# Performance work log

Hardware: AMD Instinct MI355X
Metric: run time of the kernel (lower is better)

The kernel has to match this reference:

```python
import jax, jax.numpy as jnp
import numpy as np

LN_EPS = 1e-5
GN_EPS = 0.00064
H_HEADS = 14
N_LAYER = 2

FLOATS = ["emb","ln0_w","ln0_b","ln1_w","ln1_b","ln2_w","ln2_b",
          "x_r","x_w","x_k","x_v","x_a","x_g",
          "w0","w1","w2","a0","a1","a2","v0","v1","v2","g1","g2",
          "k_k","k_a","r_k","Wr","Wk","Wv","Wo","lnx_w","lnx_b",
          "f_xk","f_key","f_val","lnout_w","lnout_b","head_w"]


def _ln(x, w, b):
    m = x.mean(-1, keepdims=True)
    v = jnp.var(x, axis=-1, keepdims=True)
    return (x - m) / jnp.sqrt(v + LN_EPS) * w + b


def _shift(x):
    # ZeroPad2d((0,0,1,-1)): token t sees token t-1, zeros at t=0
    return jnp.pad(x, ((0, 0), (1, 0), (0, 0)))[:, :-1]


def _group_norm(x, w, b, H):
    B, T, C = x.shape
    N = C // H
    xg = x.reshape(B, T, H, N)
    m = xg.mean(-1, keepdims=True)
    v = jnp.var(xg, axis=-1, keepdims=True)
    xg = (xg - m) / jnp.sqrt(v + GN_EPS)
    return xg.reshape(B, T, C) * w + b


def _rwkv7(r, w_raw, k, v, a, b, H):
    # WindBackstepping math: S_t = S_{t-1}*diag(exp(-exp(w))) + (S_{t-1} a) b^T + v k^T ; y_t = S_t r
    B, T, C = r.shape
    N = C // H
    rs = lambda t: jnp.swapaxes(t.reshape(B, T, H, N), 0, 1)  # [T,B,H,N]
    decay = jnp.exp(-jnp.exp(w_raw))
    xs = (rs(r), rs(decay), rs(k), rs(v), rs(a), rs(b))
    s0 = jnp.zeros((B, H, N, N), r.dtype)

    def step(s, inp):
        r_t, d_t, k_t, v_t, a_t, b_t = inp
        sa = jnp.einsum('bhij,bhj->bhi', s, a_t)
        s = s * d_t[:, :, None, :] + sa[..., None] * b_t[:, :, None, :] + v_t[..., None] * k_t[:, :, None, :]
        y = jnp.einsum('bhij,bhj->bhi', s, r_t)
        return s, y

    _, ys = jax.lax.scan(step, s0, xs)
    return jnp.swapaxes(ys, 0, 1).reshape(B, T, C)


def _forward(idx, P):
    H, L = H_HEADS, N_LAYER
    x = P["emb"][idx]  # [B,T,C]
    B, T, C = x.shape
    N = C // H
    v_first = jnp.zeros_like(x)
    for l in range(L):
        if l == 0:
            x = _ln(x, P["ln0_w"], P["ln0_b"])
        # --- time mix (RWKV_Tmix_x070) ---
        xn = _ln(x, P["ln1_w"][l], P["ln1_b"][l])
        xx = _shift(xn) - xn
        xr = xn + xx * P["x_r"][l]; xw = xn + xx * P["x_w"][l]
        xk = xn + xx * P["x_k"][l]; xv = xn + xx * P["x_v"][l]
        xa = xn + xx * P["x_a"][l]; xg = xn + xx * P["x_g"][l]
        r = xr @ P["Wr"][l]
        w = -jax.nn.softplus(-(P["w0"][l] + jnp.tanh(xw @ P["w1"][l]) @ P["w2"][l])) - 0.5
        k = xk @ P["Wk"][l]
        v = xv @ P["Wv"][l]
        if l == 0:
            v_first = v
        else:
            v = v + (v_first - v) * jax.nn.sigmoid(P["v0"][l] + (xv @ P["v1"][l]) @ P["v2"][l])
        a = jax.nn.sigmoid(P["a0"][l] + (xa @ P["a1"][l]) @ P["a2"][l])
        g = jax.nn.sigmoid(xg @ P["g1"][l]) @ P["g2"][l]
        kk = k * P["k_k"][l]
        kkh = kk.reshape(B, T, H, N)
        kk = (kkh / jnp.maximum(jnp.linalg.norm(kkh, axis=-1, keepdims=True), 1e-12)).reshape(B, T, C)
        k = k * (1.0 + (a - 1.0) * P["k_a"][l])
        y = _rwkv7(r, w, k, v, -kk, kk * a, H)
        y = _group_norm(y, P["lnx_w"][l], P["lnx_b"][l], H)
        rk = (r.reshape(B, T, H, N) * k.reshape(B, T, H, N) * P["r_k"][l]).sum(-1, keepdims=True)
        y = y + (rk * v.reshape(B, T, H, N)).reshape(B, T, C)
        x = x + (y * g) @ P["Wo"][l]
        # --- channel mix (RWKV_CMix_x070) ---
        xn2 = _ln(x, P["ln2_w"][l], P["ln2_b"][l])
        dx = _shift(xn2) - xn2
        kx = xn2 + dx * P["f_xk"][l]
        h = jnp.square(jax.nn.relu(kx @ P["f_key"][l]))
        x = x + h @ P["f_val"][l]
    x = _ln(x, P["lnout_w"], P["lnout_b"])
    return x @ P["head_w"]


def setup_inputs() -> dict:
    C, H, L = 896, 14, 2
    V, B, T = 32000, 4, 512
    D, DG, F4 = 64, 160, 4 * C  # LoRA dims per code formulas for C=896
    key = jax.random.key(0)
    ks = jax.random.split(key, 64)
    it = iter(range(64))

    def rn(shape, s=0.02):
        return jax.random.normal(ks[next(it)], shape, jnp.float32) * s

    def ru(shape):
        return jax.random.uniform(ks[next(it)], shape, dtype=jnp.float32)

    inp = {
        "idx": jax.random.randint(ks[next(it)], (B, T), 0, V),
        "emb": rn((V, C), 0.5),
        "ln0_w": jnp.ones((C,), jnp.float32), "ln0_b": jnp.zeros((C,), jnp.float32),
        "ln1_w": jnp.ones((L, C), jnp.float32), "ln1_b": jnp.zeros((L, C), jnp.float32),
        "ln2_w": jnp.ones((L, C), jnp.float32), "ln2_b": jnp.zeros((L, C), jnp.float32),
        "x_r": ru((L, C)), "x_w": ru((L, C)), "x_k": ru((L, C)),
        "x_v": ru((L, C)), "x_a": ru((L, C)), "x_g": ru((L, C)),
        "w0": rn((L, C), 1.0) - 2.0, "w1": rn((L, C, D)), "w2": rn((L, D, C), 0.1),
        "a0": rn((L, C), 0.1), "a1": rn((L, C, D)), "a2": rn((L, D, C), 0.1),
        "v0": rn((L, C), 0.1) + 0.73, "v1": rn((L, C, D)), "v2": rn((L, D, C), 0.1),
        "g1": rn((L, C, DG)), "g2": rn((L, DG, C), 0.1),
        "k_k": rn((L, C), 0.1) + 0.71, "k_a": rn((L, C), 0.02) + 1.02,
        "r_k": rn((L, H, C // H), 0.1) - 0.04,
        "Wr": rn((L, C, C)), "Wk": rn((L, C, C)), "Wv": rn((L, C, C)), "Wo": rn((L, C, C)),
        "lnx_w": jnp.ones((L, C), jnp.float32), "lnx_b": jnp.zeros((L, C), jnp.float32),
        "f_xk": ru((L, C)),
        "f_key": rn((L, C, F4)), "f_val": rn((L, F4, C)),
        "lnout_w": jnp.ones((C,), jnp.float32), "lnout_b": jnp.zeros((C,), jnp.float32),
        "head_w": rn((C, 1)),
    }
    return inp


def reference(idx, emb, ln0_w, ln0_b, ln1_w, ln1_b, ln2_w, ln2_b, x_r, x_w, x_k, x_v, x_a, x_g, w0, w1, w2, a0, a1, a2, v0, v1, v2, g1, g2, k_k, k_a, r_k, Wr, Wk, Wv, Wo, lnx_w, lnx_b, f_xk, f_key, f_val, lnout_w, lnout_b, head_w):
    vals = [emb, ln0_w, ln0_b, ln1_w, ln1_b, ln2_w, ln2_b, x_r, x_w, x_k, x_v, x_a, x_g, w0, w1, w2, a0, a1, a2, v0, v1, v2, g1, g2, k_k, k_a, r_k, Wr, Wk, Wv, Wo, lnx_w, lnx_b, f_xk, f_key, f_val, lnout_w, lnout_b, head_w]
    return _forward(idx, dict(zip(FLOATS, vals)))
```

## Files before the change

### kernel.cpp

```cpp
#include <hip/hip_runtime.h>
#include <hip/hip_bf16.h>
#include <math.h>

#define CC 896
#define TT 512
#define BB 4
#define HH 14
#define NN 64
#define DD 64
#define DGG 160
#define FF4 3584
#define MM (BB*TT)
#define RD 8
#define NCH 16
#define CL 32

typedef __attribute__((ext_vector_type(8))) short bf16x8;
typedef __attribute__((ext_vector_type(4))) float f32x4;

__device__ __forceinline__ float waveRedSum(float x) {
#pragma unroll
  for (int off = 32; off > 0; off >>= 1) x += __shfl_xor(x, off, 64);
  return x;
}

__device__ __forceinline__ float sigmoidf_(float x) { return 1.f / (1.f + expf(-x)); }

__device__ __forceinline__ ushort bf16bits(float v) {
  __hip_bfloat16 h = __float2bfloat16(v);
  return *(ushort*)&h;
}

__device__ __forceinline__ void gload_lds16(const void* g, void* l) {
  __builtin_amdgcn_global_load_lds((const __attribute__((address_space(1))) void*)g,
                                   (__attribute__((address_space(3))) void*)l, 16, 0, 0);
}
// ... 138 lines not shown
__device__ __forceinline__ void convT_body(const float* __restrict__ W,
                                           __hip_bfloat16* __restrict__ Wt,
                                           int K, int N, int KP, int NP,
                                           int bx, int by)
{
  __shared__ float tile[32][33];
  int bn = bx * 32, bk = by * 32;
  int tx = threadIdx.x & 31, ty = threadIdx.x >> 5;
#pragma unroll
  for (int i = 0; i < 4; i++) {
    int k = bk + ty + i * 8, n = bn + tx;
    tile[ty + i * 8][tx] = (k < K && n < N) ? W[(size_t)k * N + n] : 0.f;
  }
  __syncthreads();
#pragma unroll
  for (int i = 0; i < 4; i++) {
    int n = bn + ty + i * 8, k = bk + tx;
    if (n < NP && k < KP)
      Wt[(size_t)n * KP + k] = __float2bfloat16(tile[tx][ty + i * 8]);
  }
}

__global__ __launch_bounds__(256)
void convT_batch(const float* Wr, const float* Wk, const float* Wv, const float* Wo,
                 const float* a1, const float* a2, const float* v1, const float* v2,
                 const float* g1, const float* g2, const float* w1, const float* w2,
                 __hip_bfloat16* WrT, __hip_bfloat16* WkT, __hip_bfloat16* WvT,
                 __hip_bfloat16* WoT, __hip_bfloat16* a1T, __hip_bfloat16* a2T,
                 __hip_bfloat16* v1T, __hip_bfloat16* v2T, __hip_bfloat16* g1T,
                 __hip_bfloat16* g2T, __hip_bfloat16* w1T, __hip_bfloat16* w2T)
{
  const float* W; __hip_bfloat16* Wt; int K, N, KP, NP;
  switch (blockIdx.z) {
    case 0:  W = Wr; Wt = WrT; K = CC;  N = CC;  KP = CC;  NP = CC;  break;
    case 1:  W = Wk; Wt = WkT; K = CC;  N = CC;  KP = CC;  NP = CC;  break;
    case 2:  W = Wv; Wt = WvT; K = CC;  N = CC;  KP = CC;  NP = CC;  break;
    case 3:  W = Wo; Wt = WoT; K = CC;  N = CC;  KP = CC;  NP = CC;  break;
    case 4:  W = a1; Wt = a1T; K = CC;  N = DD;  KP = CC;  NP = DD;  break;
    case 5:  W = a2; Wt = a2T; K = DD;  N = CC;  KP = DD;  NP = CC;  break;
    case 6:  W = v1; Wt = v1T; K = CC;  N = DD;  KP = CC;  NP = DD;  break;
    case 7:  W = v2; Wt = v2T; K = DD;  N = CC;  KP = DD;  NP = CC;  break;
    case 8:  W = g1; Wt = g1T; K = CC;  N = DGG; KP = CC;  NP = 192; break;
    case 9:  W = g2; Wt = g2T; K = DGG; N = CC;  KP = 192; NP = CC;  break;
    case 10: W = w1; Wt = w1T; K = CC;  N = DD;  KP = CC;  NP = DD;  break;
    default: W = w2; Wt = w2T; K = DD;  N = CC;  KP = DD;  NP = CC;  break;
  }
  if ((int)blockIdx.x * 32 >= NP || (int)blockIdx.y * 32 >= KP) return;
  convT_body(W, Wt, K, N, KP, NP, blockIdx.x, blockIdx.y);
}

__global__ __launch_bounds__(256)
void convT_big(const float* fk, const float* fv,
               __hip_bfloat16* fkT, __hip_bfloat16* fvT)
{
  if (blockIdx.z == 0)
    convT_body(fk, fkT, CC, FF4, CC, FF4, blockIdx.x, blockIdx.y);
  else
    convT_body(fv, fvT, FF4, CC, FF4, CC, blockIdx.y, blockIdx.x);
}

template<int BN>
__device__ __forceinline__ void gemm_body(const __hip_bfloat16* __restrict__ A,
    const __hip_bfloat16* __restrict__ Bt, float* __restrict__ C,
    __hip_bfloat16* __restrict__ Cbf, int N, int K, const float* __restrict__ bias,
    const float* __restrict__ aux0, const float* __restrict__ aux1, int Nreal,
    int bx, int by, int epi)
{
  constexpr int WN = BN / 64;
  constexpr int WM = 4 / WN;
  constexpr int ROWS = 128 / WM;
  constexpr int MI = ROWS / 16;
  constexpr int BUF = (128 + BN) * 64;
  __shared__ __align__(16) ushort ldsu[2 * BUF];
  int tid = threadIdx.x;
  int lane = tid & 63, wave = tid >> 6;
  int wm, wn;
  if constexpr (WN == 2) { wm = wave >> 1; wn = wave & 1; } else { wm = wave; wn = 0; }
  int fl = lane & 15, fh = lane >> 4;
  int row0 = by * 128, col0 = bx * BN;

  const char* Abase = (const char*)A + (size_t)row0 * (size_t)(K * 2);
  const char* Bbase = (const char*)Bt + (size_t)col0 * (size_t)(K * 2);

  f32x4 acc[MI][4];
#pragma unroll
  for (int mi = 0; mi < MI; mi++)
#pragma unroll
    for (int ni = 0; ni < 4; ni++)
      acc[mi][ni] = (f32x4){0.f, 0.f, 0.f, 0.f};

  int srow = tid >> 3;
  int scol = (tid & 7) << 4;
  int ldsw = (wave << 10);

  auto stage = [&](int p, int k0) {
    char* AsB = (char*)(ldsu + p * BUF);
// ... 76 lines not shown
      int row = idx / BN;
      int col = idx - row * BN;
      float4 v4 = *(const float4*)&ldsu[idx];
      *(float4*)((char*)Cbf + ((size_t)(row0 + row) * N + col0 + col) * 2) = v4;
    }
  } else {
#pragma unroll
    for (int mi = 0; mi < MI; mi++) {
      int crow0 = row0 + wm * ROWS + mi * 16 + fh * 4;
#pragma unroll
      for (int ni = 0; ni < 4; ni++) {
        int ccol = col0 + wn * 64 + ni * 16 + fl;
#pragma unroll
        for (int e = 0; e < 4; e++) {
          size_t off = (size_t)(crow0 + e) * N + ccol;
          float v = acc[mi][ni][e];
          switch (epi) {
            case 0: C[off] = v; break;
            case 1: C[off] += v; break;
            case 5: C[off] = sigmoidf_(bias[ccol] + v); break;
            case 6: { float sg = sigmoidf_(bias[ccol] + v);
                      float vv = aux0[off];
                      C[off] = vv + (aux1[off] - vv) * sg; } break;
            default: { float z_ = bias[ccol] + v;
                       float sp_ = fmaxf(-z_, 0.f) + log1pf(expf(-fabsf(z_)));
                       C[off] = expf(-expf(-sp_ - 0.5f)); } break;
          }
        }
      }
    }
  }
}

template<int BN>
__global__ __launch_bounds__(256)
void gemm_ep(const __hip_bfloat16* __restrict__ A, const __hip_bfloat16* __restrict__ Bt,
             float* __restrict__ C, __hip_bfloat16* __restrict__ Cbf,
             int N, int K, const float* __restrict__ bias,
             const float* __restrict__ aux0, const float* __restrict__ aux1,
             int Nreal, int epi)
{
  gemm_body<BN>(A, Bt, C, Cbf, N, K, bias, aux0, aux1, Nreal, blockIdx.x, blockIdx.y, epi);
}

__global__ __launch_bounds__(256)
void gemm_rkv(const __hip_bfloat16* Ar, const __hip_bfloat16* Ak, const __hip_bfloat16* Av,
              const __hip_bfloat16* Br, const __hip_bfloat16* Bk, const __hip_bfloat16* Bv,
              float* Cr, float* Ck, float* Cv)
{
  const __hip_bfloat16* A; const __hip_bfloat16* Bt; float* C;
  if (blockIdx.z == 0)      { A = Ar; Bt = Br; C = Cr; }
  else if (blockIdx.z == 1) { A = Ak; Bt = Bk; C = Ck; }
  else                      { A = Av; Bt = Bv; C = Cv; }
  gemm_body<128>(A, Bt, C, nullptr, CC, CC, nullptr, nullptr, nullptr, CC,
                 blockIdx.x, blockIdx.y, 0);
}

__global__ __launch_bounds__(256)
void lora1_batch(const __hip_bfloat16* mixw, const __hip_bfloat16* mixa,
                 const __hip_bfloat16* mixv, const __hip_bfloat16* mixg,
                 const __hip_bfloat16* w1T, const __hip_bfloat16* a1T,
                 const __hip_bfloat16* v1T, const __hip_bfloat16* g1T,
                 __hip_bfloat16* t64w, __hip_bfloat16* t64a,
                 __hip_bfloat16* t64v, __hip_bfloat16* t160)
{
  int z = blockIdx.x;
  const __hip_bfloat16 *A, *Bt; __hip_bfloat16* Cbf; int N, epi, bx, Nreal;
  if (z == 0)      { A = mixw; Bt = w1T; Cbf = t64w; N = 64;  epi = 8; bx = 0; Nreal = 64; }
  else if (z == 1) { A = mixa; Bt = a1T; Cbf = t64a; N = 64;  epi = 3; bx = 0; Nreal = 64; }
  else if (z == 2) { A = mixv; Bt = v1T; Cbf = t64v; N = 64;  epi = 3; bx = 0; Nreal = 64; }
  else             { A = mixg; Bt = g1T; Cbf = t160; N = 192; epi = 4; bx = z - 3; Nreal = DGG; }
  gemm_body<64>(A, Bt, nullptr, Cbf, N, CC, nullptr, nullptr, nullptr, Nreal,
                bx, blockIdx.y, epi);
}

__global__ __launch_bounds__(256)
void lora2_batch(const __hip_bfloat16* t64w, const __hip_bfloat16* t64a,
                 const __hip_bfloat16* t160, const __hip_bfloat16* t64v,
                 const __hip_bfloat16* w2T, const __hip_bfloat16* a2T,
                 const __hip_bfloat16* g2T, const __hip_bfloat16* v2T,
                 float* dcy, float* ab, float* gb, float* vb,
                 const float* w0l, const float* a0l, const float* v0l,
                 const float* vfirst)
{
  int z = blockIdx.z;
  const __hip_bfloat16 *A, *Bt; float* C; const float* bias;
  const float *ax0, *ax1; int K, epi;
  if (z == 0)      { A = t64w; Bt = w2T; C = dcy; bias = w0l; K = 64;  epi = 7; ax0 = nullptr; ax1 = nullptr; }
  else if (z == 1) { A = t64a; Bt = a2T; C = ab;  bias = a0l; K = 64;  epi = 5; ax0 = nullptr; ax1 = nullptr; }
  else if (z == 2) { A = t160; Bt = g2T; C = gb;  bias = nullptr; K = 192; epi = 0; ax0 = nullptr; ax1 = nullptr; }
  else             { A = t64v; Bt = v2T; C = vb;  bias = v0l; K = 64;  epi = 6; ax0 = vb; ax1 = vfirst; }
  gemm_body<128>(A, Bt, C, nullptr, CC, K, bias, ax0, ax1, CC, blockIdx.x, blockIdx.y, epi);
}

__global__ __launch_bounds__(896)
void prep_kernel(const float* __restrict__ k_in, const float* __restrict__ a,
                 const float* __restrict__ k_k, const float* __restrict__ k_a,
                 float* __restrict__ kout, float* __restrict__ ain, float* __restrict__ bin)
{
  int m = blockIdx.x;
  int c = threadIdx.x;
  size_t off = (size_t)m * CC + c;
  float kv = k_in[off];
  float av = a[off];
  float kkv = kv * k_k[c];
  float ss = waveRedSum(kkv * kkv);
  float norm = sqrtf(ss);
  float kkn = kkv / fmaxf(norm, 1e-12f);
  ain[off] = -kkn;
  bin[off] = kkn * av;
  kout[off] = kv * (1.f + (av - 1.f) * k_a[c]);
}

__global__ __launch_bounds__(256)
void scanp1_kernel(const float* __restrict__ rp, const float* __restrict__ dp,
                   const float* __restrict__ kp, const float* __restrict__ vp,
                   const float* __restrict__ ap, const float* __restrict__ bp_,
                   float* __restrict__ yp, float* __restrict__ ubuf,
                   float* __restrict__ Pc, float* __restrict__ Zc)
{
  int bid = blockIdx.x;
  int bh = bid >> 4, c = bid & 15;
  int b = bh / HH, h = bh - b * HH;
  int tid = threadIdx.x, lane = tid & 63, w = tid >> 6;
  int w16 = w * 16;
  __shared__ __align__(16) float ring[RD][6][64];
  __shared__ float sa_part[2][4][64];
  __shared__ float pa_part[2][4][64];
  __shared__ float y_part[2][4][64];
  __shared__ float u_part[2][4][64];

  float s[16], p[16];
#pragma unroll
  for (int jj = 0; jj < 16; jj++) {
    s[jj] = 0.f;
    p[jj] = (lane == w16 + jj) ? 1.f : 0.f;
  }
  size_t base = ((size_t)b * TT + (size_t)c * CL) * CC + (size_t)h * NN + lane;

  const float* gA = nullptr; const float* gB = nullptr; int slA = 0, slB = 0;
  if (w == 1)      { gA = rp;  slA = 0; gB = dp;  slB = 1; }
  else if (w == 2) { gA = kp;  slA = 2; gB = vp;  slB = 5; }
  else if (w == 3) { gA = ap;  slA = 3; gB = bp_; slB = 4; }

  if (w) {
    for (int t0 = 0; t0 < RD; t0++) {
      gload_lds4(gA + base + (size_t)t0 * CC, &ring[t0][slA][0]);
      gload_lds4(gB + base + (size_t)t0 * CC, &ring[t0][slB][0]);
    }
    asm volatile("s_waitcnt vmcnt(0)" ::: "memory");
  }
  __builtin_amdgcn_s_barrier();
  __builtin_amdgcn_sched_barrier(0);

  for (int t = 0; t < CL; ++t) {
    int Pp = t & 1, Qp = Pp ^ 1;
    int slot = t & (RD - 1);
    float av[16], dv[16], kv[16], bv[16], rv[16];
#pragma unroll
    for (int q = 0; q < 4; q++) {
      *(float4*)&av[q * 4] = *(const float4*)&ring[slot][3][w16 + q * 4];
      *(float4*)&dv[q * 4] = *(const float4*)&ring[slot][1][w16 + q * 4];
      *(float4*)&kv[q * 4] = *(const float4*)&ring[slot][2][w16 + q * 4];
      *(float4*)&bv[q * 4] = *(const float4*)&ring[slot][4][w16 + q * 4];
      *(float4*)&rv[q * 4] = *(const float4*)&ring[slot][0][w16 + q * 4];
    }
    float vi = ring[slot][5][lane];
    float sp0 = 0.f, sp1 = 0.f, pp0 = 0.f, pp1 = 0.f;
#pragma unroll
    for (int jj = 0; jj < 8; jj++) {
      sp0 = fmaf(s[jj],     av[jj],     sp0);
      sp1 = fmaf(s[jj + 8], av[jj + 8], sp1);
      pp0 = fmaf(p[jj],     av[jj],     pp0);
      pp1 = fmaf(p[jj + 8], av[jj + 8], pp1);
    }
    sa_part[Pp][w][lane] = sp0 + sp1;
    pa_part[Pp][w][lane] = pp0 + pp1;
    if (w) { asm volatile("s_waitcnt vmcnt(12)" ::: "memory"); }
    asm volatile("s_waitcnt lgkmcnt(0)" ::: "memory");
    __builtin_amdgcn_s_barrier();
    __builtin_amdgcn_sched_barrier(0);
    if (w && t + RD < CL) {
      gload_lds4(gA + base + (size_t)(t + RD) * CC, &ring[slot][slA][0]);
      gload_lds4(gB + base + (size_t)(t + RD) * CC, &ring[slot][slB][0]);
    }
    if (w == 0 && t > 0) {
      float yo = (y_part[Qp][0][lane] + y_part[Qp][1][lane])
               + (y_part[Qp][2][lane] + y_part[Qp][3][lane]);
      yp[base + (size_t)(t - 1) * CC] = yo;
      float uo = (u_part[Qp][0][lane] + u_part[Qp][1][lane])
               + (u_part[Qp][2][lane] + u_part[Qp][3][lane]);
      ubuf[((size_t)bid * CL + (t - 1)) * 64 + lane] = uo;
    }
    float sa = (sa_part[Pp][0][lane] + sa_part[Pp][1][lane])
             + (sa_part[Pp][2][lane] + sa_part[Pp][3][lane]);
    float pa = (pa_part[Pp][0][lane] + pa_part[Pp][1][lane])
             + (pa_part[Pp][2][lane] + pa_part[Pp][3][lane]);
    float y0 = 0.f, y1 = 0.f, u0 = 0.f, u1 = 0.f;
#pragma unroll
    for (int jj = 0; jj < 8; jj++) {
      s[jj]     = fmaf(s[jj],     dv[jj],     fmaf(sa, bv[jj],     vi * kv[jj]));
      y0 = fmaf(s[jj], rv[jj], y0);
      s[jj + 8] = fmaf(s[jj + 8], dv[jj + 8], fmaf(sa, bv[jj + 8], vi * kv[jj + 8]));
      y1 = fmaf(s[jj + 8], rv[jj + 8], y1);
      p[jj]     = fmaf(p[jj],     dv[jj],     pa * bv[jj]);
      u0 = fmaf(p[jj], rv[jj], u0);
      p[jj + 8] = fmaf(p[jj + 8], dv[jj + 8], pa * bv[jj + 8]);
      u1 = fmaf(p[jj + 8], rv[jj + 8], u1);
    }
    y_part[Pp][w][lane] = y0 + y1;
    u_part[Pp][w][lane] = u0 + u1;
  }

  asm volatile("s_waitcnt lgkmcnt(0)" ::: "memory");
  __builtin_amdgcn_s_barrier();
  if (w == 0) {
    int Pl = (CL - 1) & 1;
    float yo = (y_part[Pl][0][lane] + y_part[Pl][1][lane])
             + (y_part[Pl][2][lane] + y_part[Pl][3][lane]);
    yp[base + (size_t)(CL - 1) * CC] = yo;
    float uo = (u_part[Pl][0][lane] + u_part[Pl][1][lane])
             + (u_part[Pl][2][lane] + u_part[Pl][3][lane]);
    ubuf[((size_t)bid * CL + (CL - 1)) * 64 + lane] = uo;
  }
  float* zp = Zc + ((size_t)bid * 64 + lane) * 64 + w16;
  float* pq = Pc + ((size_t)bid * 64 + lane) * 64 + w16;
#pragma unroll
  for (int q = 0; q < 4; q++) {
    *(float4*)&zp[q * 4] = make_float4(s[q*4], s[q*4+1], s[q*4+2], s[q*4+3]);
    *(float4*)&pq[q * 4] = make_float4(p[q*4], p[q*4+1], p[q*4+2], p[q*4+3]);
  }
}

__global__ __launch_bounds__(512)
void scanp2_kernel(const float* __restrict__ Pc, const float* __restrict__ Zc,
                   float* __restrict__ Sin)
{
  int bh = blockIdx.x;
  int tid = threadIdx.x;
  int i = tid & 63, jg = tid >> 6, j0 = jg * 8;
  int sr = tid >> 3, sq = (tid & 7) * 8;
  __shared__ float S_lds[64][65];
  __shared__ __align__(16) float P_lds[64][68];

#pragma unroll
  for (int jj = 0; jj < 8; jj++) S_lds[i][j0 + jj] = 0.f;

  size_t b0 = (size_t)bh * NCH * 4096;
  float4 pr0 = *(const float4*)(Pc + b0 + (size_t)sr * 64 + sq);
  float4 pr1 = *(const float4*)(Pc + b0 + (size_t)sr * 64 + sq + 4);

  for (int c = 0; c < NCH; c++) {
    size_t bidc = (size_t)bh * NCH + c;
// ... 117 lines not shown
  const float* v1     = (const float*)d_in[21];
  const float* v2     = (const float*)d_in[22];
  const float* g1     = (const float*)d_in[23];
  const float* g2     = (const float*)d_in[24];
  const float* k_k    = (const float*)d_in[25];
  const float* k_a    = (const float*)d_in[26];
  const float* r_k    = (const float*)d_in[27];
  const float* Wr     = (const float*)d_in[28];
  const float* Wk     = (const float*)d_in[29];
  const float* Wv     = (const float*)d_in[30];
  const float* Wo     = (const float*)d_in[31];
  const float* lnx_w  = (const float*)d_in[32];
  const float* lnx_b  = (const float*)d_in[33];
  const float* f_xk   = (const float*)d_in[34];
  const float* f_key  = (const float*)d_in[35];
  const float* f_val  = (const float*)d_in[36];
  const float* lnout_w = (const float*)d_in[37];
  const float* lnout_b = (const float*)d_in[38];
  const float* head_w  = (const float*)d_in[39];
  float* out = (float*)d_out;

  const size_t MC = (size_t)MM * CC;
  const size_t W2 = (size_t)CC * CC;
  float* ws   = (float*)d_ws;
  float* x      = ws;
  float* vfirst = x + MC;
  float* rb     = vfirst + MC;
  float* dcy    = rb + MC;
  float* kb     = dcy + MC;
  float* vb     = kb + MC;
  float* ab     = vb + MC;
  float* gb     = ab + MC;
  float* ainb   = gb + MC;
  float* binb   = ainb + MC;
  float* yb     = binb + MC;
  float* ubuf   = yb + MC;
  float* Pcb    = ubuf + MC;
  float* Zcb    = Pcb + 2 * MC;
  float* Sinb   = Zcb + 2 * MC;
  float* fend   = Sinb + 2 * MC;

  __hip_bfloat16* mixr_bf = (__hip_bfloat16*)fend;
  __hip_bfloat16* mixw_bf = mixr_bf + MC;
  __hip_bfloat16* mixk_bf = mixw_bf + MC;
  __hip_bfloat16* mixv_bf = mixk_bf + MC;
  __hip_bfloat16* mixa_bf = mixv_bf + MC;
  __hip_bfloat16* mixg_bf = mixa_bf + MC;
  __hip_bfloat16* WrT = mixg_bf + MC;
  __hip_bfloat16* WkT = WrT + W2;
  __hip_bfloat16* WvT = WkT + W2;
  __hip_bfloat16* WoT = WvT + W2;
  __hip_bfloat16* fkT = WoT + W2;
  __hip_bfloat16* fvT = fkT + (size_t)FF4 * CC;
  __hip_bfloat16* w1T = fvT + (size_t)FF4 * CC;
  __hip_bfloat16* a1T = w1T + (size_t)DD * CC;
  __hip_bfloat16* v1T = a1T + (size_t)DD * CC;
  __hip_bfloat16* w2T = v1T + (size_t)DD * CC;
  __hip_bfloat16* a2T = w2T + (size_t)DD * CC;
  __hip_bfloat16* v2T = a2T + (size_t)DD * CC;
  __hip_bfloat16* g1T = v2T + (size_t)DD * CC;
  __hip_bfloat16* g2T = g1T + (size_t)192 * CC;
  __hip_bfloat16* t64w = g2T + (size_t)192 * CC;
  __hip_bfloat16* t64a = t64w + (size_t)MM * 64;
  __hip_bfloat16* t64v = t64a + (size_t)MM * 64;
  __hip_bfloat16* t160 = t64v + (size_t)MM * 64;
  __hip_bfloat16* h_bf  = (__hip_bfloat16*)rb;
  __hip_bfloat16* yg_bf = (__hip_bfloat16*)ab;

  dim3 blk(256);

  ln_kernel<<<MM, blk, 0, stream>>>(emb, idx, ln0_w, ln0_b, x);

  for (int l = 0; l < 2; l++) {
    const float* Wr_l = Wr + (size_t)l * W2;
    const float* Wk_l = Wk + (size_t)l * W2;
    const float* Wv_l = Wv + (size_t)l * W2;
    const float* Wo_l = Wo + (size_t)l * W2;
    const float* w1_l = w1 + (size_t)l * CC * DD;
    const float* w2_l = w2 + (size_t)l * DD * CC;
    const float* a1_l = a1 + (size_t)l * CC * DD;
    const float* a2_l = a2 + (size_t)l * DD * CC;
    const float* v1_l = v1 + (size_t)l * CC * DD;
    const float* v2_l = v2 + (size_t)l * DD * CC;
    const float* g1_l = g1 + (size_t)l * CC * DGG;
    const float* g2_l = g2 + (size_t)l * DGG * CC;
    const float* fk_l = f_key + (size_t)l * CC * FF4;
    const float* fv_l = f_val + (size_t)l * FF4 * CC;

    convT_batch<<<dim3(28, 28, 12), blk, 0, stream>>>(
        Wr_l, Wk_l, Wv_l, Wo_l, a1_l, a2_l, v1_l, v2_l, g1_l, g2_l, w1_l, w2_l,
        WrT, WkT, WvT, WoT, a1T, a2T, v1T, v2T, g1T, g2T, w1T, w2T);
    convT_big<<<dim3(112, 28, 2), blk, 0, stream>>>(fk_l, fv_l, fkT, fvT);

    lnmix6_kernel<<<MM, blk, 0, stream>>>(x, ln1_w + l * CC, ln1_b + l * CC,
        x_r + l * CC, x_w + l * CC, x_k + l * CC, x_v + l * CC, x_a + l * CC, x_g + l * CC,
        mixr_bf, mixw_bf, mixk_bf, mixv_bf, mixa_bf, mixg_bf);

    gemm_rkv<<<dim3(7, 16, 3), blk, 0, stream>>>(mixr_bf, mixk_bf, mixv_bf,
                                                 WrT, WkT, WvT, rb, kb, vb);
    if (l == 0)
      hipMemcpyAsync(vfirst, vb, MC * sizeof(float), hipMemcpyDeviceToDevice, stream);

    lora1_batch<<<dim3(6, 16), blk, 0, stream>>>(mixw_bf, mixa_bf, mixv_bf, mixg_bf,
                                                 w1T, a1T, v1T, g1T,
                                                 t64w, t64a, t64v, t160);
    lora2_batch<<<dim3(7, 16, l == 0 ? 3 : 4), blk, 0, stream>>>(
        t64w, t64a, t160, t64v, w2T, a2T, g2T, v2T,
        dcy, ab, gb, vb, w0 + l * CC, a0 + l * CC, v0 + l * CC, vfirst);

    prep_kernel<<<MM, dim3(896), 0, stream>>>(kb, ab, k_k + l * CC, k_a + l * CC,
                                              kb, ainb, binb);
    scanp1_kernel<<<BB * HH * NCH, blk, 0, stream>>>(rb, dcy, kb, vb, ainb, binb,
                                                     yb, ubuf, Pcb, Zcb);
    scanp2_kernel<<<BB * HH, dim3(512), 0, stream>>>(Pcb, Zcb, Sinb);
    scanp3gn_kernel<<<BB * HH * NCH, blk, 0, stream>>>(Sinb, ubuf, yb, rb, kb, vb, gb,
        lnx_w + l * CC, lnx_b + l * CC, r_k + (size_t)l * CC, yg_bf);

    gemm_ep<64><<<dim3(14, 16), blk, 0, stream>>>(yg_bf, WoT, x, nullptr, CC, CC,
                                                  nullptr, nullptr, nullptr, CC, 1);

    lnmixc_kernel<<<MM, blk, 0, stream>>>(x, ln2_w + l * CC, ln2_b + l * CC,
                                          f_xk + l * CC, mixr_bf);
    gemm_ep<128><<<dim3(28, 16), blk, 0, stream>>>(mixr_bf, fkT, nullptr, h_bf, FF4, CC,
                                                   nullptr, nullptr, nullptr, FF4, 2);
    gemm_ep<64><<<dim3(14, 16), blk, 0, stream>>>(h_bf, fvT, x, nullptr, CC, FF4,
                                                  nullptr, nullptr, nullptr, CC, 1);
  }

  head_kernel<<<MM, blk, 0, stream>>>(x, lnout_w, lnout_b, head_w, out);
}
```

Before: 759.6 us.

## Batch weight conversion, fuse rkv and lora1 GEMMs, restructure chunk scan

Weight transposition for both layers now runs once, up front, in two launches, using per-layer weight buffers. The r/k/v GEMM and the first LoRA GEMMs are merged into one launch, and the v_first copy is folded into a GEMM epilogue in place of a separate memcpy. The chunk-scan phase-1 kernel is rewritten so each wave owns 16 state rows split across lane quads. It reduces with cross-lane shuffles instead of LDS partial sums and barriers, and loads inputs in double-buffered 8-step batches. Costs are a larger workspace and a merged kernel that holds the larger LDS allocation for all of its blocks.

```diff
diff --git a/kernel.cpp b/kernel.cpp
--- a/kernel.cpp
+++ b/kernel.cpp
@@ -11,7 +11,6 @@
 #define DGG 160
 #define FF4 3584
 #define MM (BB*TT)
-#define RD 8
 #define NCH 16
 #define CL 32
 
@@ -196,56 +195,59 @@
 }
 
 __global__ __launch_bounds__(256)
-void convT_batch(const float* Wr, const float* Wk, const float* Wv, const float* Wo,
-                 const float* a1, const float* a2, const float* v1, const float* v2,
-                 const float* g1, const float* g2, const float* w1, const float* w2,
-                 __hip_bfloat16* WrT, __hip_bfloat16* WkT, __hip_bfloat16* WvT,
-                 __hip_bfloat16* WoT, __hip_bfloat16* a1T, __hip_bfloat16* a2T,
-                 __hip_bfloat16* v1T, __hip_bfloat16* v2T, __hip_bfloat16* g1T,
-                 __hip_bfloat16* g2T, __hip_bfloat16* w1T, __hip_bfloat16* w2T)
-{
+void convT_batch2(const float* Wr, const float* Wk, const float* Wv, const float* Wo,
+                  const float* a1, const float* a2, const float* v1, const float* v2,
+                  const float* g1, const float* g2, const float* w1, const float* w2,
+                  __hip_bfloat16* WrT, __hip_bfloat16* WkT, __hip_bfloat16* WvT,
+                  __hip_bfloat16* WoT, __hip_bfloat16* a1T, __hip_bfloat16* a2T,
+                  __hip_bfloat16* v1T, __hip_bfloat16* v2T, __hip_bfloat16* g1T,
+                  __hip_bfloat16* g2T, __hip_bfloat16* w1T, __hip_bfloat16* w2T)
+{
+  int l = blockIdx.z / 12, idx = blockIdx.z % 12;
+  const size_t W2 = (size_t)CC * CC, WD = (size_t)DD * CC, WG = (size_t)192 * CC;
   const float* W; __hip_bfloat16* Wt; int K, N, KP, NP;
-  switch (blockIdx.z) {
-    case 0:  W = Wr; Wt = WrT; K = CC;  N = CC;  KP = CC;  NP = CC;  break;
-    case 1:  W = Wk; Wt = WkT; K = CC;  N = CC;  KP = CC;  NP = CC;  break;
-    case 2:  W = Wv; Wt = WvT; K = CC;  N = CC;  KP = CC;  NP = CC;  break;
-    case 3:  W = Wo; Wt = WoT; K = CC;  N = CC;  KP = CC;  NP = CC;  break;
-    case 4:  W = a1; Wt = a1T; K = CC;  N = DD;  KP = CC;  NP = DD;  break;
-    case 5:  W = a2; Wt = a2T; K = DD;  N = CC;  KP = DD;  NP = CC;  break;
-    case 6:  W = v1; Wt = v1T; K = CC;  N = DD;  KP = CC;  NP = DD;  break;
-    case 7:  W = v2; Wt = v2T; K = DD;  N = CC;  KP = DD;  NP = CC;  break;
-    case 8:  W = g1; Wt = g1T; K = CC;  N = DGG; KP = CC;  NP = 192; break;
-    case 9:  W = g2; Wt = g2T; K = DGG; N = CC;  KP = 192; NP = CC;  break;
-    case 10: W = w1; Wt = w1T; K = CC;  N = DD;  KP = CC;  NP = DD;  break;
-    default: W = w2; Wt = w2T; K = DD;  N = CC;  KP = DD;  NP = CC;  break;
+  switch (idx) {
+    case 0:  W = Wr + l*W2;          Wt = WrT + l*W2; K = CC;  N = CC;  KP = CC;  NP = CC;  break;
+    case 1:  W = Wk + l*W2;          Wt = WkT + l*W2; K = CC;  N = CC;  KP = CC;  NP = CC;  break;
+    case 2:  W = Wv + l*W2;          Wt = WvT + l*W2; K = CC;  N = CC;  KP = CC;  NP = CC;  break;
+    case 3:  W = Wo + l*W2;          Wt = WoT + l*W2; K = CC;  N = CC;  KP = CC;  NP = CC;  break;
+    case 4:  W = a1 + l*WD;          Wt = a1T + l*WD; K = CC;  N = DD;  KP = CC;  NP = DD;  break;
+    case 5:  W = a2 + l*WD;          Wt = a2T + l*WD; K = DD;  N = CC;  KP = DD;  NP = CC;  break;
+    case 6:  W = v1 + l*WD;          Wt = v1T + l*WD; K = CC;  N = DD;  KP = CC;  NP = DD;  break;
+    case 7:  W = v2 + l*WD;          Wt = v2T + l*WD; K = DD;  N = CC;  KP = DD;  NP = CC;  break;
+    case 8:  W = g1 + l*(size_t)CC*DGG; Wt = g1T + l*WG; K = CC;  N = DGG; KP = CC;  NP = 192; break;
+    case 9:  W = g2 + l*(size_t)CC*DGG; Wt = g2T + l*WG; K = DGG; N = CC;  KP = 192; NP = CC;  break;
+    case 10: W = w1 + l*WD;          Wt = w1T + l*WD; K = CC;  N = DD;  KP = CC;  NP = DD;  break;
+    default: W = w2 + l*WD;          Wt = w2T + l*WD; K = DD;  N = CC;  KP = DD;  NP = CC;  break;
   }
   if ((int)blockIdx.x * 32 >= NP || (int)blockIdx.y * 32 >= KP) return;
   convT_body(W, Wt, K, N, KP, NP, blockIdx.x, blockIdx.y);
 }
 
 __global__ __launch_bounds__(256)
-void convT_big(const float* fk, const float* fv,
-               __hip_bfloat16* fkT, __hip_bfloat16* fvT)
-{
-  if (blockIdx.z == 0)
-    convT_body(fk, fkT, CC, FF4, CC, FF4, blockIdx.x, blockIdx.y);
+void convT_big2(const float* fk, const float* fv,
+                __hip_bfloat16* fkT, __hip_bfloat16* fvT)
+{
+  int l = blockIdx.z >> 1, which = blockIdx.z & 1;
+  const size_t WF = (size_t)FF4 * CC;
+  if (which == 0)
+    convT_body(fk + l*WF, fkT + l*WF, CC, FF4, CC, FF4, blockIdx.x, blockIdx.y);
   else
-    convT_body(fv, fvT, FF4, CC, FF4, CC, blockIdx.y, blockIdx.x);
+    convT_body(fv + l*WF, fvT + l*WF, FF4, CC, FF4, CC, blockIdx.y, blockIdx.x);
 }
 
 template<int BN>
 __device__ __forceinline__ void gemm_body(const __hip_bfloat16* __restrict__ A,
     const __hip_bfloat16* __restrict__ Bt, float* __restrict__ C,
     __hip_bfloat16* __restrict__ Cbf, int N, int K, const float* __restrict__ bias,
-    const float* __restrict__ aux0, const float* __restrict__ aux1, int Nreal,
-    int bx, int by, int epi)
+    const float* __restrict__ aux0, const float* __restrict__ aux1,
+    float* __restrict__ auxw, int Nreal, int bx, int by, int epi, ushort* ldsu)
 {
   constexpr int WN = BN / 64;
   constexpr int WM = 4 / WN;
   constexpr int ROWS = 128 / WM;
   constexpr int MI = ROWS / 16;
   constexpr int BUF = (128 + BN) * 64;
-  __shared__ __align__(16) ushort ldsu[2 * BUF];
   int tid = threadIdx.x;
   int lane = tid & 63, wave = tid >> 6;
   int wm, wn;
@@ -368,6 +370,7 @@
             case 6: { float sg = sigmoidf_(bias[ccol] + v);
                       float vv = aux0[off];
                       C[off] = vv + (aux1[off] - vv) * sg; } break;
+            case 9: C[off] = v; auxw[off] = v; break;
             default: { float z_ = bias[ccol] + v;
                        float sp_ = fmaxf(-z_, 0.f) + log1pf(expf(-fabsf(z_)));
                        C[off] = expf(-expf(-sp_ - 0.5f)); } break;
@@ -386,38 +389,42 @@
              const float* __restrict__ aux0, const float* __restrict__ aux1,
              int Nreal, int epi)
 {
-  gemm_body<BN>(A, Bt, C, Cbf, N, K, bias, aux0, aux1, Nreal, blockIdx.x, blockIdx.y, epi);
-}
-
-__global__ __launch_bounds__(256)
-void gemm_rkv(const __hip_bfloat16* Ar, const __hip_bfloat16* Ak, const __hip_bfloat16* Av,
-              const __hip_bfloat16* Br, const __hip_bfloat16* Bk, const __hip_bfloat16* Bv,
-              float* Cr, float* Ck, float* Cv)
-{
-  const __hip_bfloat16* A; const __hip_bfloat16* Bt; float* C;
-  if (blockIdx.z == 0)      { A = Ar; Bt = Br; C = Cr; }
-  else if (blockIdx.z == 1) { A = Ak; Bt = Bk; C = Ck; }
-  else                      { A = Av; Bt = Bv; C = Cv; }
-  gemm_body<128>(A, Bt, C, nullptr, CC, CC, nullptr, nullptr, nullptr, CC,
-                 blockIdx.x, blockIdx.y, 0);
-}
-
-__global__ __launch_bounds__(256)
-void lora1_batch(const __hip_bfloat16* mixw, const __hip_bfloat16* mixa,
-                 const __hip_bfloat16* mixv, const __hip_bfloat16* mixg,
-                 const __hip_bfloat16* w1T, const __hip_bfloat16* a1T,
-                 const __hip_bfloat16* v1T, const __hip_bfloat16* g1T,
-                 __hip_bfloat16* t64w, __hip_bfloat16* t64a,
-                 __hip_bfloat16* t64v, __hip_bfloat16* t160)
-{
-  int z = blockIdx.x;
-  const __hip_bfloat16 *A, *Bt; __hip_bfloat16* Cbf; int N, epi, bx, Nreal;
-  if (z == 0)      { A = mixw; Bt = w1T; Cbf = t64w; N = 64;  epi = 8; bx = 0; Nreal = 64; }
-  else if (z == 1) { A = mixa; Bt = a1T; Cbf = t64a; N = 64;  epi = 3; bx = 0; Nreal = 64; }
-  else if (z == 2) { A = mixv; Bt = v1T; Cbf = t64v; N = 64;  epi = 3; bx = 0; Nreal = 64; }
-  else             { A = mixg; Bt = g1T; Cbf = t160; N = 192; epi = 4; bx = z - 3; Nreal = DGG; }
-  gemm_body<64>(A, Bt, nullptr, Cbf, N, CC, nullptr, nullptr, nullptr, Nreal,
-                bx, blockIdx.y, epi);
+  __shared__ __align__(16) ushort lds[2 * (128 + BN) * 64];
+  gemm_body<BN>(A, Bt, C, Cbf, N, K, bias, aux0, aux1, nullptr, Nreal,
+                blockIdx.x, blockIdx.y, epi, lds);
+}
+
+__global__ __launch_bounds__(256)
+void gemm_rkv_lora1(const __hip_bfloat16* Ar, const __hip_bfloat16* Ak, const __hip_bfloat16* Av,
+                    const __hip_bfloat16* mixw, const __hip_bfloat16* mixa, const __hip_bfloat16* mixg,
+                    const __hip_bfloat16* Br, const __hip_bfloat16* Bk, const __hip_bfloat16* Bv,
+                    const __hip_bfloat16* w1T, const __hip_bfloat16* a1T,
+                    const __hip_bfloat16* v1T, const __hip_bfloat16* g1T,
+                    float* Cr, float* Ck, float* Cv, float* vfirst,
+                    __hip_bfloat16* t64w, __hip_bfloat16* t64a,
+                    __hip_bfloat16* t64v, __hip_bfloat16* t160, int copy_vfirst)
+{
+  __shared__ __align__(16) ushort lds[2 * (128 + 128) * 64];
+  int z = blockIdx.z;
+  if (z < 3) {
+    const __hip_bfloat16 *A, *Bt; float* C; int epi = 0; float* aw = nullptr;
+    if (z == 0)      { A = Ar; Bt = Br; C = Cr; }
+    else if (z == 1) { A = Ak; Bt = Bk; C = Ck; }
+    else             { A = Av; Bt = Bv; C = Cv;
+                       if (copy_vfirst) { epi = 9; aw = vfirst; } }
+    gemm_body<128>(A, Bt, C, nullptr, CC, CC, nullptr, nullptr, nullptr, aw, CC,
+                   blockIdx.x, blockIdx.y, epi, lds);
+  } else {
+    int bx = blockIdx.x;
+    if (bx >= 6) return;
+    const __hip_bfloat16 *A, *Bt; __hip_bfloat16* Cbf; int N, epi, bxx, Nreal;
+    if (bx == 0)      { A = mixw; Bt = w1T; Cbf = t64w; N = 64;  epi = 8; bxx = 0; Nreal = 64; }
+    else if (bx == 1) { A = mixa; Bt = a1T; Cbf = t64a; N = 64;  epi = 3; bxx = 0; Nreal = 64; }
+    else if (bx == 2) { A = Av;   Bt = v1T; Cbf = t64v; N = 64;  epi = 3; bxx = 0; Nreal = 64; }
+    else              { A = mixg; Bt = g1T; Cbf = t160; N = 192; epi = 4; bxx = bx - 3; Nreal = DGG; }
+    gemm_body<64>(A, Bt, nullptr, Cbf, N, CC, nullptr, nullptr, nullptr, nullptr, Nreal,
+                  bxx, blockIdx.y, epi, lds);
+  }
 }
 
 __global__ __launch_bounds__(256)
@@ -429,6 +436,7 @@
                  const float* w0l, const float* a0l, const float* v0l,
                  const float* vfirst)
 {
+  __shared__ __align__(16) ushort lds[2 * (128 + 128) * 64];
   int z = blockIdx.z;
   const __hip_bfloat16 *A, *Bt; float* C; const float* bias;
   const float *ax0, *ax1; int K, epi;
@@ -436,7 +444,8 @@
   else if (z == 1) { A = t64a; Bt = a2T; C = ab;  bias = a0l; K = 64;  epi = 5; ax0 = nullptr; ax1 = nullptr; }
   else if (z == 2) { A = t160; Bt = g2T; C = gb;  bias = nullptr; K = 192; epi = 0; ax0 = nullptr; ax1 = nullptr; }
   else             { A = t64v; Bt = v2T; C = vb;  bias = v0l; K = 64;  epi = 6; ax0 = vb; ax1 = vfirst; }
-  gemm_body<128>(A, Bt, C, nullptr, CC, K, bias, ax0, ax1, CC, blockIdx.x, blockIdx.y, epi);
+  gemm_body<128>(A, Bt, C, nullptr, CC, K, bias, ax0, ax1, nullptr, CC,
+                 blockIdx.x, blockIdx.y, epi, lds);
 }
 
 __global__ __launch_bounds__(896)
@@ -459,7 +468,7 @@
 }
 
 __global__ __launch_bounds__(256)
-void scanp1_kernel(const float* __restrict__ rp, const float* __restrict__ dp,
+void scanrs_kernel(const float* __restrict__ rp, const float* __restrict__ dp,
                    const float* __restrict__ kp, const float* __restrict__ vp,
                    const float* __restrict__ ap, const float* __restrict__ bp_,
                    float* __restrict__ yp, float* __restrict__ ubuf,
@@ -469,112 +478,97 @@
   int bh = bid >> 4, c = bid & 15;
   int b = bh / HH, h = bh - b * HH;
   int tid = threadIdx.x, lane = tid & 63, w = tid >> 6;
-  int w16 = w * 16;
-  __shared__ __align__(16) float ring[RD][6][64];
-  __shared__ float sa_part[2][4][64];
-  __shared__ float pa_part[2][4][64];
-  __shared__ float y_part[2][4][64];
-  __shared__ float u_part[2][4][64];
+  int rl = lane & 15, quad = lane >> 4;
+  int row = w * 16 + rl;
+  int col0 = quad * 16;
+  __shared__ __align__(16) float ring[2][8][6][64];
 
   float s[16], p[16];
 #pragma unroll
   for (int jj = 0; jj < 16; jj++) {
     s[jj] = 0.f;
-    p[jj] = (lane == w16 + jj) ? 1.f : 0.f;
-  }
-  size_t base = ((size_t)b * TT + (size_t)c * CL) * CC + (size_t)h * NN + lane;
-
-  const float* gA = nullptr; const float* gB = nullptr; int slA = 0, slB = 0;
-  if (w == 1)      { gA = rp;  slA = 0; gB = dp;  slB = 1; }
-  else if (w == 2) { gA = kp;  slA = 2; gB = vp;  slB = 5; }
-  else if (w == 3) { gA = ap;  slA = 3; gB = bp_; slB = 4; }
-
-  if (w) {
-    for (int t0 = 0; t0 < RD; t0++) {
-      gload_lds4(gA + base + (size_t)t0 * CC, &ring[t0][slA][0]);
-      gload_lds4(gB + base + (size_t)t0 * CC, &ring[t0][slB][0]);
-    }
-    asm volatile("s_waitcnt vmcnt(0)" ::: "memory");
-  }
-  __builtin_amdgcn_s_barrier();
-  __builtin_amdgcn_sched_barrier(0);
-
-  for (int t = 0; t < CL; ++t) {
-    int Pp = t & 1, Qp = Pp ^ 1;
-    int slot = t & (RD - 1);
-    float av[16], dv[16], kv[16], bv[16], rv[16];
-#pragma unroll
-    for (int q = 0; q < 4; q++) {
-      *(float4*)&av[q * 4] = *(const float4*)&ring[slot][3][w16 + q * 4];
-      *(float4*)&dv[q * 4] = *(const float4*)&ring[slot][1][w16 + q * 4];
-      *(float4*)&kv[q * 4] = *(const float4*)&ring[slot][2][w16 + q * 4];
-      *(float4*)&bv[q * 4] = *(const float4*)&ring[slot][4][w16 + q * 4];
-      *(float4*)&rv[q * 4] = *(const float4*)&ring[slot][0][w16 + q * 4];
-    }
-    float vi = ring[slot][5][lane];
-    float sp0 = 0.f, sp1 = 0.f, pp0 = 0.f, pp1 = 0.f;
-#pragma unroll
-    for (int jj = 0; jj < 8; jj++) {
-      sp0 = fmaf(s[jj],     av[jj],     sp0);
-      sp1 = fmaf(s[jj + 8], av[jj + 8], sp1);
-      pp0 = fmaf(p[jj],     av[jj],     pp0);
-      pp1 = fmaf(p[jj + 8], av[jj + 8], pp1);
-    }
-    sa_part[Pp][w][lane] = sp0 + sp1;
-    pa_part[Pp][w][lane] = pp0 + pp1;
-    if (w) { asm volatile("s_waitcnt vmcnt(12)" ::: "memory"); }
-    asm volatile("s_waitcnt lgkmcnt(0)" ::: "memory");
+    p[jj] = (col0 + jj == row) ? 1.f : 0.f;
+  }
+  size_t cbase = ((size_t)b * TT + (size_t)c * CL) * CC + (size_t)h * NN;
+
+  auto issueL = [&](int q) {
+    int rr = q & 1;
+#pragma unroll
+    for (int k2 = 0; k2 < 2; ++k2) {
+      int st = 2 * w + k2;
+      size_t o = cbase + (size_t)(q * 8 + st) * CC + lane;
+      gload_lds4(rp + o,  &ring[rr][st][0][0]);
+      gload_lds4(dp + o,  &ring[rr][st][1][0]);
+      gload_lds4(kp + o,  &ring[rr][st][2][0]);
+      gload_lds4(ap + o,  &ring[rr][st][3][0]);
+      gload_lds4(bp_ + o, &ring[rr][st][4][0]);
+      gload_lds4(vp + o,  &ring[rr][st][5][0]);
+    }
+  };
+
+  issueL(0);
+  for (int q = 0; q < CL / 8; ++q) {
+    if (q == 0) asm volatile("s_waitcnt vmcnt(0)" ::: "memory");
+    else        asm volatile("s_waitcnt vmcnt(16)" ::: "memory");
     __builtin_amdgcn_s_barrier();
     __builtin_amdgcn_sched_barrier(0);
-    if (w && t + RD < CL) {
-      gload_lds4(gA + base + (size_t)(t + RD) * CC, &ring[slot][slA][0]);
-      gload_lds4(gB + base + (size_t)(t + RD) * CC, &ring[slot][slB][0]);
-    }
-    if (w == 0 && t > 0) {
-      float yo = (y_part[Qp][0][lane] + y_part[Qp][1][lane])
-               + (y_part[Qp][2][lane] + y_part[Qp][3][lane]);
-      yp[base + (size_t)(t - 1) * CC] = yo;
-      float uo = (u_part[Qp][0][lane] + u_part[Qp][1][lane])
-               + (u_part[Qp][2][lane] + u_part[Qp][3][lane]);
-      ubuf[((size_t)bid * CL + (t - 1)) * 64 + lane] = uo;
-    }
-    float sa = (sa_part[Pp][0][lane] + sa_part[Pp][1][lane])
-             + (sa_part[Pp][2][lane] + sa_part[Pp][3][lane]);
-    float pa = (pa_part[Pp][0][lane] + pa_part[Pp][1][lane])
-             + (pa_part[Pp][2][lane] + pa_part[Pp][3][lane]);
-    float y0 = 0.f, y1 = 0.f, u0 = 0.f, u1 = 0.f;
-#pragma unroll
-    for (int jj = 0; jj < 8; jj++) {
-      s[jj]     = fmaf(s[jj],     dv[jj],     fmaf(sa, bv[jj],     vi * kv[jj]));
-      y0 = fmaf(s[jj], rv[jj], y0);
-      s[jj + 8] = fmaf(s[jj + 8], dv[jj + 8], fmaf(sa, bv[jj + 8], vi * kv[jj + 8]));
-      y1 = fmaf(s[jj + 8], rv[jj + 8], y1);
-      p[jj]     = fmaf(p[jj],     dv[jj],     pa * bv[jj]);
-      u0 = fmaf(p[jj], rv[jj], u0);
-      p[jj + 8] = fmaf(p[jj + 8], dv[jj + 8], pa * bv[jj + 8]);
-      u1 = fmaf(p[jj + 8], rv[jj + 8], u1);
-    }
-    y_part[Pp][w][lane] = y0 + y1;
-    u_part[Pp][w][lane] = u0 + u1;
-  }
-
-  asm volatile("s_waitcnt lgkmcnt(0)" ::: "memory");
-  __builtin_amdgcn_s_barrier();
-  if (w == 0) {
-    int Pl = (CL - 1) & 1;
-    float yo = (y_part[Pl][0][lane] + y_part[Pl][1][lane])
-             + (y_part[Pl][2][lane] + y_part[Pl][3][lane]);
-    yp[base + (size_t)(CL - 1) * CC] = yo;
-    float uo = (u_part[Pl][0][lane] + u_part[Pl][1][lane])
-             + (u_part[Pl][2][lane] + u_part[Pl][3][lane]);
-    ubuf[((size_t)bid * CL + (CL - 1)) * 64 + lane] = uo;
-  }
-  float* zp = Zc + ((size_t)bid * 64 + lane) * 64 + w16;
-  float* pq = Pc + ((size_t)bid * 64 + lane) * 64 + w16;
-#pragma unroll
-  for (int q = 0; q < 4; q++) {
-    *(float4*)&zp[q * 4] = make_float4(s[q*4], s[q*4+1], s[q*4+2], s[q*4+3]);
-    *(float4*)&pq[q * 4] = make_float4(p[q*4], p[q*4+1], p[q*4+2], p[q*4+3]);
+    if (q + 1 < CL / 8) issueL(q + 1);
+    __builtin_amdgcn_sched_barrier(0);
+    int rr = q & 1;
+#pragma unroll 2
+    for (int st = 0; st < 8; ++st) {
+      int t = q * 8 + st;
+      float rv[16], dv[16], kv[16], av[16], bv[16];
+#pragma unroll
+      for (int qd = 0; qd < 4; qd++) {
+        *(float4*)&rv[qd * 4] = *(const float4*)&ring[rr][st][0][col0 + qd * 4];
+        *(float4*)&dv[qd * 4] = *(const float4*)&ring[rr][st][1][col0 + qd * 4];
+        *(float4*)&kv[qd * 4] = *(const float4*)&ring[rr][st][2][col0 + qd * 4];
+        *(float4*)&av[qd * 4] = *(const float4*)&ring[rr][st][3][col0 + qd * 4];
+        *(float4*)&bv[qd * 4] = *(const float4*)&ring[rr][st][4][col0 + qd * 4];
+      }
+      float vi = ring[rr][st][5][row];
+      float sa0 = 0.f, sa1 = 0.f, pa0 = 0.f, pa1 = 0.f;
+#pragma unroll
+      for (int jj = 0; jj < 8; jj++) {
+        sa0 = fmaf(s[jj],     av[jj],     sa0);
+        sa1 = fmaf(s[jj + 8], av[jj + 8], sa1);
+        pa0 = fmaf(p[jj],     av[jj],     pa0);
+        pa1 = fmaf(p[jj + 8], av[jj + 8], pa1);
+      }
+      float sa = sa0 + sa1;
+      sa += __shfl_xor(sa, 16, 64); sa += __shfl_xor(sa, 32, 64);
+      float pa = pa0 + pa1;
+      pa += __shfl_xor(pa, 16, 64); pa += __shfl_xor(pa, 32, 64);
+      float y0 = 0.f, y1 = 0.f, u0 = 0.f, u1 = 0.f;
+#pragma unroll
+      for (int jj = 0; jj < 8; jj++) {
+        s[jj]     = fmaf(s[jj],     dv[jj],     fmaf(sa, bv[jj],     vi * kv[jj]));
+        y0 = fmaf(s[jj], rv[jj], y0);
+        p[jj]     = fmaf(p[jj],     dv[jj],     pa * bv[jj]);
+        u0 = fmaf(p[jj], rv[jj], u0);
+        s[jj + 8] = fmaf(s[jj + 8], dv[jj + 8], fmaf(sa, bv[jj + 8], vi * kv[jj + 8]));
+        y1 = fmaf(s[jj + 8], rv[jj + 8], y1);
+        p[jj + 8] = fmaf(p[jj + 8], dv[jj + 8], pa * bv[jj + 8]);
+        u1 = fmaf(p[jj + 8], rv[jj + 8], u1);
+      }
+      float yv_ = y0 + y1;
+      yv_ += __shfl_xor(yv_, 16, 64); yv_ += __shfl_xor(yv_, 32, 64);
+      float uv_ = u0 + u1;
+      uv_ += __shfl_xor(uv_, 16, 64); uv_ += __shfl_xor(uv_, 32, 64);
+      if (quad == 0) {
+        yp[cbase + (size_t)t * CC + row] = yv_;
+        ubuf[((size_t)bid * CL + t) * 64 + row] = uv_;
+      }
+    }
+  }
+
+  float* zp = Zc + ((size_t)bid * 64 + row) * 64 + col0;
+  float* pq = Pc + ((size_t)bid * 64 + row) * 64 + col0;
+#pragma unroll
+  for (int q4 = 0; q4 < 4; q4++) {
+    *(float4*)&zp[q4 * 4] = make_float4(s[q4*4], s[q4*4+1], s[q4*4+2], s[q4*4+3]);
+    *(float4*)&pq[q4 * 4] = make_float4(p[q4*4], p[q4*4+1], p[q4*4+2], p[q4*4+3]);
   }
 }
 
@@ -738,6 +732,9 @@
 
   const size_t MC = (size_t)MM * CC;
   const size_t W2 = (size_t)CC * CC;
+  const size_t WD = (size_t)DD * CC;
+  const size_t WG = (size_t)192 * CC;
+  const size_t WF = (size_t)FF4 * CC;
   float* ws   = (float*)d_ws;
   float* x      = ws;
   float* vfirst = x + MC;
@@ -763,20 +760,20 @@
   __hip_bfloat16* mixa_bf = mixv_bf + MC;
   __hip_bfloat16* mixg_bf = mixa_bf + MC;
   __hip_bfloat16* WrT = mixg_bf + MC;
-  __hip_bfloat16* WkT = WrT + W2;
-  __hip_bfloat16* WvT = WkT + W2;
-  __hip_bfloat16* WoT = WvT + W2;
-  __hip_bfloat16* fkT = WoT + W2;
-  __hip_bfloat16* fvT = fkT + (size_t)FF4 * CC;
-  __hip_bfloat16* w1T = fvT + (size_t)FF4 * CC;
-  __hip_bfloat16* a1T = w1T + (size_t)DD * CC;
-  __hip_bfloat16* v1T = a1T + (size_t)DD * CC;
-  __hip_bfloat16* w2T = v1T + (size_t)DD * CC;
-  __hip_bfloat16* a2T = w2T + (size_t)DD * CC;
-  __hip_bfloat16* v2T = a2T + (size_t)DD * CC;
-  __hip_bfloat16* g1T = v2T + (size_t)DD * CC;
-  __hip_bfloat16* g2T = g1T + (size_t)192 * CC;
-  __hip_bfloat16* t64w = g2T + (size_t)192 * CC;
+  __hip_bfloat16* WkT = WrT + 2 * W2;
+  __hip_bfloat16* WvT = WkT + 2 * W2;
+  __hip_bfloat16* WoT = WvT + 2 * W2;
+  __hip_bfloat16* fkT = WoT + 2 * W2;
+  __hip_bfloat16* fvT = fkT + 2 * WF;
+  __hip_bfloat16* w1T = fvT + 2 * WF;
+  __hip_bfloat16* a1T = w1T + 2 * WD;
+  __hip_bfloat16* v1T = a1T + 2 * WD;
+  __hip_bfloat16* w2T = v1T + 2 * WD;
+  __hip_bfloat16* a2T = w2T + 2 * WD;
+  __hip_bfloat16* v2T = a2T + 2 * WD;
+  __hip_bfloat16* g1T = v2T + 2 * WD;
+  __hip_bfloat16* g2T = g1T + 2 * WG;
+  __hip_bfloat16* t64w = g2T + 2 * WG;
   __hip_bfloat16* t64a = t64w + (size_t)MM * 64;
   __hip_bfloat16* t64v = t64a + (size_t)MM * 64;
   __hip_bfloat16* t160 = t64v + (size_t)MM * 64;
@@ -785,61 +782,45 @@
 
   dim3 blk(256);
 
+  convT_batch2<<<dim3(28, 28, 24), blk, 0, stream>>>(
+      Wr, Wk, Wv, Wo, a1, a2, v1, v2, g1, g2, w1, w2,
+      WrT, WkT, WvT, WoT, a1T, a2T, v1T, v2T, g1T, g2T, w1T, w2T);
+  convT_big2<<<dim3(112, 28, 4), blk, 0, stream>>>(f_key, f_val, fkT, fvT);
+
   ln_kernel<<<MM, blk, 0, stream>>>(emb, idx, ln0_w, ln0_b, x);
 
   for (int l = 0; l < 2; l++) {
-    const float* Wr_l = Wr + (size_t)l * W2;
-    const float* Wk_l = Wk + (size_t)l * W2;
-    const float* Wv_l = Wv + (size_t)l * W2;
-    const float* Wo_l = Wo + (size_t)l * W2;
-    const float* w1_l = w1 + (size_t)l * CC * DD;
-    const float* w2_l = w2 + (size_t)l * DD * CC;
-    const float* a1_l = a1 + (size_t)l * CC * DD;
-    const float* a2_l = a2 + (size_t)l * DD * CC;
-    const float* v1_l = v1 + (size_t)l * CC * DD;
-    const float* v2_l = v2 + (size_t)l * DD * CC;
-    const float* g1_l = g1 + (size_t)l * CC * DGG;
-    const float* g2_l = g2 + (size_t)l * DGG * CC;
-    const float* fk_l = f_key + (size_t)l * CC * FF4;
-    const float* fv_l = f_val + (size_t)l * FF4 * CC;
-
-    convT_batch<<<dim3(28, 28, 12), blk, 0, stream>>>(
-        Wr_l, Wk_l, Wv_l, Wo_l, a1_l, a2_l, v1_l, v2_l, g1_l, g2_l, w1_l, w2_l,
-        WrT, WkT, WvT, WoT, a1T, a2T, v1T, v2T, g1T, g2T, w1T, w2T);
-    convT_big<<<dim3(112, 28, 2), blk, 0, stream>>>(fk_l, fv_l, fkT, fvT);
-
     lnmix6_kernel<<<MM, blk, 0, stream>>>(x, ln1_w + l * CC, ln1_b + l * CC,
         x_r + l * CC, x_w + l * CC, x_k + l * CC, x_v + l * CC, x_a + l * CC, x_g + l * CC,
         mixr_bf, mixw_bf, mixk_bf, mixv_bf, mixa_bf, mixg_bf);
 
-    gemm_rkv<<<dim3(7, 16, 3), blk, 0, stream>>>(mixr_bf, mixk_bf, mixv_bf,
-                                                 WrT, WkT, WvT, rb, kb, vb);
-    if (l == 0)
-      hipMemcpyAsync(vfirst, vb, MC * sizeof(float), hipMemcpyDeviceToDevice, stream);
-
-    lora1_batch<<<dim3(6, 16), blk, 0, stream>>>(mixw_bf, mixa_bf, mixv_bf, mixg_bf,
-                                                 w1T, a1T, v1T, g1T,
-                                                 t64w, t64a, t64v, t160);
+    gemm_rkv_lora1<<<dim3(7, 16, 4), blk, 0, stream>>>(
+        mixr_bf, mixk_bf, mixv_bf, mixw_bf, mixa_bf, mixg_bf,
+        WrT + l * W2, WkT + l * W2, WvT + l * W2,
+        w1T + l * WD, a1T + l * WD, v1T + l * WD, g1T + l * WG,
+        rb, kb, vb, vfirst, t64w, t64a, t64v, t160, l == 0 ? 1 : 0);
+
     lora2_batch<<<dim3(7, 16, l == 0 ? 3 : 4), blk, 0, stream>>>(
-        t64w, t64a, t160, t64v, w2T, a2T, g2T, v2T,
+        t64w, t64a, t160, t64v,
+        w2T + l * WD, a2T + l * WD, g2T + l * WG, v2T + l * WD,
         dcy, ab, gb, vb, w0 + l * CC, a0 + l * CC, v0 + l * CC, vfirst);
 
     prep_kernel<<<MM, dim3(896), 0, stream>>>(kb, ab, k_k + l * CC, k_a + l * CC,
                                               kb, ainb, binb);
-    scanp1_kernel<<<BB * HH * NCH, blk, 0, stream>>>(rb, dcy, kb, vb, ainb, binb,
+    scanrs_kernel<<<BB * HH * NCH, blk, 0, stream>>>(rb, dcy, kb, vb, ainb, binb,
                                                      yb, ubuf, Pcb, Zcb);
     scanp2_kernel<<<BB * HH, dim3(512), 0, stream>>>(Pcb, Zcb, Sinb);
     scanp3gn_kernel<<<BB * HH * NCH, blk, 0, stream>>>(Sinb, ubuf, yb, rb, kb, vb, gb,
         lnx_w + l * CC, lnx_b + l * CC, r_k + (size_t)l * CC, yg_bf);
 
-    gemm_ep<64><<<dim3(14, 16), blk, 0, stream>>>(yg_bf, WoT, x, nullptr, CC, CC,
+    gemm_ep<64><<<dim3(14, 16), blk, 0, stream>>>(yg_bf, WoT + l * W2, x, nullptr, CC, CC,
                                                   nullptr, nullptr, nullptr, CC, 1);
 
     lnmixc_kernel<<<MM, blk, 0, stream>>>(x, ln2_w + l * CC, ln2_b + l * CC,
                                           f_xk + l * CC, mixr_bf);
-    gemm_ep<128><<<dim3(28, 16), blk, 0, stream>>>(mixr_bf, fkT, nullptr, h_bf, FF4, CC,
-                                                   nullptr, nullptr, nullptr, FF4, 2);
-    gemm_ep<64><<<dim3(14, 16), blk, 0, stream>>>(h_bf, fvT, x, nullptr, CC, FF4,
+    gemm_ep<128><<<dim3(28, 16), blk, 0, stream>>>(mixr_bf, fkT + l * WF, nullptr, h_bf,
+                                                   FF4, CC, nullptr, nullptr, nullptr, FF4, 2);
+    gemm_ep<64><<<dim3(14, 16), blk, 0, stream>>>(h_bf, fvT + l * WF, x, nullptr, CC, FF4,
                                                   nullptr, nullptr, nullptr, CC, 1);
   }
 
```

After: 697.9 us. -8.1%, faster.
